# Optimization experiments

Measured on AMD Instinct MI355X. Metric: run time of the kernel, lower is better.

Reference implementation:

```python
import jax, jax.numpy as jnp
import numpy as np

H = 15  # hidden_dim


def _lstm_layer(x_seq, w_ih, w_hh, b_ih, b_hh):
    """One LSTM layer, PyTorch gate order (i, f, g, o).
    x_seq: (T, B, D_in) -> returns output sequence (T, B, H)."""
    T, B, _ = x_seq.shape
    # Precompute input contribution for all timesteps at once: (T, B, 4H)
    xw = jnp.einsum('tbd,gd->tbg', x_seq, w_ih) + b_ih + b_hh

    def step(carry, xw_t):
        h, c = carry
        gates = xw_t + h @ w_hh.T  # (B, 4H)
        i, f, g, o = jnp.split(gates, 4, axis=-1)
        i = jax.nn.sigmoid(i)
        f = jax.nn.sigmoid(f)
        g = jnp.tanh(g)
        o = jax.nn.sigmoid(o)
        c = f * c + i * g
        h = o * jnp.tanh(c)
        return (h, c), h

    h0 = jnp.zeros((B, H), dtype=x_seq.dtype)
    c0 = jnp.zeros((B, H), dtype=x_seq.dtype)
    _, out = jax.lax.scan(step, (h0, c0), xw)
    return out  # (T, B, H)


def setup_inputs() -> dict:
    key = jax.random.key(0)
    ks = jax.random.split(key, 11)
    D, OUT = 5, 25
    s = 0.1
    return {
        'x':     jax.random.normal(ks[0], (512, 4096, D), dtype=jnp.float32),
        'w_ih0': jax.random.normal(ks[1], (4 * H, D), dtype=jnp.float32) * s,
        'w_hh0': jax.random.normal(ks[2], (4 * H, H), dtype=jnp.float32) * s,
        'b_ih0': jax.random.normal(ks[3], (4 * H,), dtype=jnp.float32) * s,
        'b_hh0': jax.random.normal(ks[4], (4 * H,), dtype=jnp.float32) * s,
        'w_ih1': jax.random.normal(ks[5], (4 * H, H), dtype=jnp.float32) * s,
        'w_hh1': jax.random.normal(ks[6], (4 * H, H), dtype=jnp.float32) * s,
        'b_ih1': jax.random.normal(ks[7], (4 * H,), dtype=jnp.float32) * s,
        'b_hh1': jax.random.normal(ks[8], (4 * H,), dtype=jnp.float32) * s,
        'w_lin': jax.random.normal(ks[9], (OUT, H), dtype=jnp.float32) * s,
        'b_lin': jax.random.normal(ks[10], (OUT,), dtype=jnp.float32) * s,
    }


def reference(x, w_ih0, w_hh0, b_ih0, b_hh0, w_ih1, w_hh1, b_ih1, b_hh1, w_lin, b_lin):
    out0 = _lstm_layer(x, w_ih0, w_hh0, b_ih0, b_hh0)      # (T, B, H)
    out1 = _lstm_layer(out0, w_ih1, w_hh1, b_ih1, b_hh1)   # (T, B, H)
    # Faithful to the source: output[:, -1, :] with seq-first layout selects
    # the last BATCH element across all timesteps -> (T, H)
    last = out1[:, -1, :]
    return last @ w_lin.T + b_lin  # (T, OUT)
```

## Files before the change

kernel.cpp:

```cpp
#include <hip/hip_runtime.h>

#define T_SEQ 512
#define BATCH 4096
#define D_IN  5
#define H     15
#define G4    60
#define OUTN  25

#define LOG2E   1.4426950408889634f
#define M_SIG  (-1.4426950408889634f)
#define M_TANH (-2.8853901f)

__device__ __forceinline__ float fast_exp2(float x) {
#if __has_builtin(__builtin_amdgcn_exp2f)
  return __builtin_amdgcn_exp2f(x);
#else
  return exp2f(x);
#endif
}

__device__ __forceinline__ float fast_rcp(float x) {
#if __has_builtin(__builtin_amdgcn_rcpf)
  return __builtin_amdgcn_rcpf(x);
#else
  return 1.0f / x;
#endif
}

__device__ __forceinline__ float rl(float v, int lane) {
  return __int_as_float(__builtin_amdgcn_readlane(__float_as_int(v), lane));
}

template <int K>
__device__ __forceinline__ float qbcast(float v) {
  return __int_as_float(__builtin_amdgcn_update_dpp(
      0, __float_as_int(v), K * 0x55, 0xF, 0xF, true));
}

__global__ void precompute_xw0(const float* __restrict__ x,
                               const float* __restrict__ w_ih0,
                               const float* __restrict__ b_ih0,
                               const float* __restrict__ b_hh0,
                               float* __restrict__ xw0) {
  int idx = blockIdx.x * blockDim.x + threadIdx.x;
  if (idx >= T_SEQ * G4) return;
  int t = idx / G4;
  int g = idx - t * G4;
  const float* xp = x + ((size_t)t * BATCH + (BATCH - 1)) * D_IN;
  float a = b_ih0[g] + b_hh0[g];
#pragma unroll
  for (int d = 0; d < D_IN; ++d) a = fmaf(xp[d], w_ih0[g * D_IN + d], a);
  float m = (g / H == 2) ? M_TANH : M_SIG;
  xw0[idx] = a * m;
}

__global__ void __launch_bounds__(64, 1)
lstm_serial(const float* __restrict__ xw0,
            const float* __restrict__ w_hh0,
            const float* __restrict__ w_ih1,
            const float* __restrict__ w_hh1,
            const float* __restrict__ b_ih1,
            const float* __restrict__ b_hh1,
            const float* __restrict__ w_lin,
            const float* __restrict__ b_lin,
            float* __restrict__ out) {
  const int lane = threadIdx.x;
  const int ty = lane & 3;
  const int j  = lane >> 2;
  const int g  = (j < H) ? (ty * H + j) : 0;

  const bool  isT = (ty == 2);
  const float m   = isT ? M_TANH : M_SIG;
  const float scv  = isT ? (2.0f * M_TANH) : 1.0f;
  const float offv = isT ? (-M_TANH) : 0.0f;

  float w0[H], wi1[H], wh1[H];
#pragma unroll
  for (int k = 0; k < H; ++k) {
    w0[k]  = w_hh0[g * H + k] * m;
    wi1[k] = w_ih1[g * H + k] * m;
    wh1[k] = w_hh1[g * H + k] * m;
  }
  const float bias1 = (b_ih1[g] + b_hh1[g]) * m;

  float wl[H];
  {
    int o = (lane < OUTN) ? lane : 0;
#pragma unroll
    for (int k = 0; k < H; ++k) wl[k] = w_lin[o * H + k];
  }
  const float bl = b_lin[(lane < OUTN) ? lane : 0];

  float c0 = 0.0f, c1 = 0.0f;
  float sh0[H], sh1[H];
#pragma unroll
  for (int k = 0; k < H; ++k) { sh0[k] = 0.0f; sh1[k] = 0.0f; }

  float h0v = 0.0f, h1v = 0.0f;

  auto L0 = [&](float xw) {
    float a0 = xw, a1 = 0.0f, a2 = 0.0f;
#pragma unroll
    for (int k = 0; k < 5; ++k)   a0 = fmaf(w0[k], sh0[k], a0);
#pragma unroll
    for (int k = 5; k < 10; ++k)  a1 = fmaf(w0[k], sh0[k], a1);
#pragma unroll
    for (int k = 10; k < 15; ++k) a2 = fmaf(w0[k], sh0[k], a2);
    float a = a0 + (a1 + a2);
    float e = fast_exp2(a);
    float s = fast_rcp(1.0f + e);
    float v = fmaf(s, scv, offv);
    float vi = qbcast<0>(v), vf = qbcast<1>(v), vg = qbcast<2>(v), vo = qbcast<3>(v);
    c0 = fmaf(vf, c0, vi * vg);
    float th = fmaf(fast_rcp(1.0f + fast_exp2(c0)), 2.0f, -1.0f);
    h0v = vo * th;
  };
  auto L1 = [&]() {
    float u0 = bias1, u1 = 0.0f, u2 = 0.0f, u3 = 0.0f, u4 = 0.0f, u5 = 0.0f;
#pragma unroll
    for (int k = 0; k < 5; ++k)   { u0 = fmaf(wi1[k], sh0[k], u0); u3 = fmaf(wh1[k], sh1[k], u3); }
#pragma unroll
    for (int k = 5; k < 10; ++k)  { u1 = fmaf(wi1[k], sh0[k], u1); u4 = fmaf(wh1[k], sh1[k], u4); }
#pragma unroll
    for (int k = 10; k < 15; ++k) { u2 = fmaf(wi1[k], sh0[k], u2); u5 = fmaf(wh1[k], sh1[k], u5); }
    float b = ((u0 + u1) + (u2 + u3)) + (u4 + u5);
    float e = fast_exp2(b);
    float s = fast_rcp(1.0f + e);
    float v = fmaf(s, scv, offv);
    float qi = qbcast<0>(v), qf = qbcast<1>(v), qg = qbcast<2>(v), qo = qbcast<3>(v);
    c1 = fmaf(qf, c1, qi * qg);
    float th = fmaf(fast_rcp(1.0f + fast_exp2(c1)), 2.0f, -1.0f);
    h1v = qo * th;
  };
  auto B0 = [&]() {
#pragma unroll
    for (int k = 0; k < H; ++k) sh0[k] = rl(h0v, 4 * k);
  };
  auto B1 = [&]() {
#pragma unroll
    for (int k = 0; k < H; ++k) sh1[k] = rl(h1v, 4 * k);
  };
  auto LIN = [&](int t2, bool do_store) {
    float o0 = bl, o1 = 0.0f, o2 = 0.0f;
#pragma unroll
    for (int k = 0; k < 5; ++k)   o0 = fmaf(wl[k], sh1[k], o0);
#pragma unroll
    for (int k = 5; k < 10; ++k)  o1 = fmaf(wl[k], sh1[k], o1);
#pragma unroll
    for (int k = 10; k < 15; ++k) o2 = fmaf(wl[k], sh1[k], o2);
    if (do_store && lane < OUTN) out[t2 * OUTN + lane] = o0 + (o1 + o2);
  };

  float xw_cur = xw0[g];
  float xw_n1  = xw0[1 * G4 + g];
  L0(xw_cur);
  B0();
  xw_cur = xw_n1;
  xw_n1  = xw0[2 * G4 + g];

  for (int i = 1; i < T_SEQ; ++i) {
    int tn = (i + 2 < T_SEQ) ? (i + 2) : 0;
    float xw_n2 = xw0[tn * G4 + g];

    L1();
    L0(xw_cur);
    LIN(i - 2, i >= 2);

    B0();
    B1();

    xw_cur = xw_n1;
    xw_n1  = xw_n2;
  }

  LIN(T_SEQ - 2, true);
  L1();
  B1();
  LIN(T_SEQ - 1, true);
}

extern "C" void kernel_launch(void* const* d_in, const int* in_sizes, int n_in,
                              void* d_out, int out_size, void* d_ws, size_t ws_size,
                              hipStream_t stream) {
  const float* x     = (const float*)d_in[0];
  const float* w_ih0 = (const float*)d_in[1];
  const float* w_hh0 = (const float*)d_in[2];
  const float* b_ih0 = (const float*)d_in[3];
  const float* b_hh0 = (const float*)d_in[4];
  const float* w_ih1 = (const float*)d_in[5];
  const float* w_hh1 = (const float*)d_in[6];
  const float* b_ih1 = (const float*)d_in[7];
  const float* b_hh1 = (const float*)d_in[8];
  const float* w_lin = (const float*)d_in[9];
  const float* b_lin = (const float*)d_in[10];
  float* out = (float*)d_out;
  float* xw0 = (float*)d_ws;

  precompute_xw0<<<dim3((T_SEQ * G4 + 255) / 256), dim3(256), 0, stream>>>(
      x, w_ih0, b_ih0, b_hh0, xw0);
  lstm_serial<<<dim3(1), dim3(64), 0, stream>>>(
      xw0, w_hh0, w_ih1, w_hh1, b_ih1, b_hh1, w_lin, b_lin, out);
}
```

Measured before the change: 236.9 us.

## Split LSTM layers and linear head across three wavefronts in a barrier pipeline

Replaces the single-wavefront serial loop with a three-wave workgroup. Wave 0 runs layer 0, wave 1 runs layer 1 one step behind, and wave 2 runs the output projection, with hidden states passed through small ring buffers in shared memory. A workgroup barrier runs every step. The goal is to take layer-1 and linear work off the critical path so each wave's serial chain is shorter and the waves run concurrently. In exchange, every step now pays for a barrier, LDS writes and reads, and an lgkmcnt wait.

```diff
diff --git a/kernel.cpp b/kernel.cpp
--- a/kernel.cpp
+++ b/kernel.cpp
@@ -6,8 +6,8 @@
 #define H     15
 #define G4    60
 #define OUTN  25
-
-#define LOG2E   1.4426950408889634f
+#define NITER (T_SEQ + 4)
+
 #define M_SIG  (-1.4426950408889634f)
 #define M_TANH (-2.8853901f)
 
@@ -35,6 +35,12 @@
 __device__ __forceinline__ float qbcast(float v) {
   return __int_as_float(__builtin_amdgcn_update_dpp(
       0, __float_as_int(v), K * 0x55, 0xF, 0xF, true));
+}
+
+__device__ __forceinline__ void wg_barrier() {
+  asm volatile("s_waitcnt lgkmcnt(0)" ::: "memory");
+  __builtin_amdgcn_s_barrier();
+  asm volatile("" ::: "memory");
 }
 
 __global__ void precompute_xw0(const float* __restrict__ x,
@@ -54,129 +60,159 @@
   xw0[idx] = a * m;
 }
 
-__global__ void __launch_bounds__(64, 1)
-lstm_serial(const float* __restrict__ xw0,
-            const float* __restrict__ w_hh0,
-            const float* __restrict__ w_ih1,
-            const float* __restrict__ w_hh1,
-            const float* __restrict__ b_ih1,
-            const float* __restrict__ b_hh1,
-            const float* __restrict__ w_lin,
-            const float* __restrict__ b_lin,
-            float* __restrict__ out) {
-  const int lane = threadIdx.x;
+__global__ void __launch_bounds__(192, 1)
+lstm_pipe(const float* __restrict__ xw0,
+          const float* __restrict__ w_hh0,
+          const float* __restrict__ w_ih1,
+          const float* __restrict__ w_hh1,
+          const float* __restrict__ b_ih1,
+          const float* __restrict__ b_hh1,
+          const float* __restrict__ w_lin,
+          const float* __restrict__ b_lin,
+          float* __restrict__ out) {
+  __shared__ __align__(16) float h0buf[4][16];
+  __shared__ __align__(16) float h1buf[4][16];
+
+  const int tid  = threadIdx.x;
+  const int wid  = tid >> 6;
+  const int lane = tid & 63;
   const int ty = lane & 3;
   const int j  = lane >> 2;
   const int g  = (j < H) ? (ty * H + j) : 0;
 
-  const bool  isT = (ty == 2);
-  const float m   = isT ? M_TANH : M_SIG;
+  const bool  isT  = (ty == 2);
+  const float m    = isT ? M_TANH : M_SIG;
   const float scv  = isT ? (2.0f * M_TANH) : 1.0f;
   const float offv = isT ? (-M_TANH) : 0.0f;
 
-  float w0[H], wi1[H], wh1[H];
-#pragma unroll
-  for (int k = 0; k < H; ++k) {
-    w0[k]  = w_hh0[g * H + k] * m;
-    wi1[k] = w_ih1[g * H + k] * m;
-    wh1[k] = w_hh1[g * H + k] * m;
+  if (wid == 0) {
+    float w0[H];
+#pragma unroll
+    for (int k = 0; k < H; ++k) w0[k] = w_hh0[g * H + k] * m;
+    float sh0[H];
+#pragma unroll
+    for (int k = 0; k < H; ++k) sh0[k] = 0.0f;
+    float c0 = 0.0f;
+    float xw_cur = xw0[g];
+    float xw_n1  = xw0[G4 + g];
+
+    for (int i = 0; i < NITER; ++i) {
+      if (i < T_SEQ) {
+        int tn = (i + 2 < T_SEQ) ? (i + 2) : 0;
+        float xw_n2 = xw0[tn * G4 + g];
+
+        float a0 = xw_cur, a1 = 0.0f, a2 = 0.0f;
+#pragma unroll
+        for (int k = 0; k < 5; ++k)   a0 = fmaf(w0[k], sh0[k], a0);
+#pragma unroll
+        for (int k = 5; k < 10; ++k)  a1 = fmaf(w0[k], sh0[k], a1);
+#pragma unroll
+        for (int k = 10; k < 15; ++k) a2 = fmaf(w0[k], sh0[k], a2);
+        float a = a0 + (a1 + a2);
+        float e = fast_exp2(a);
+        float s = fast_rcp(1.0f + e);
+        float v = fmaf(s, scv, offv);
+        float vi = qbcast<0>(v), vf = qbcast<1>(v), vg = qbcast<2>(v), vo = qbcast<3>(v);
+        c0 = fmaf(vf, c0, vi * vg);
+        float th = fmaf(fast_rcp(1.0f + fast_exp2(c0)), 2.0f, -1.0f);
+        float h0v = vo * th;
+
+        if (ty == 0 && j < H) h0buf[i & 3][j] = h0v;
+#pragma unroll
+        for (int k = 0; k < H; ++k) sh0[k] = rl(h0v, 4 * k);
+
+        xw_cur = xw_n1;
+        xw_n1  = xw_n2;
+      }
+      wg_barrier();
+    }
+  } else if (wid == 1) {
+    float wi1[H], wh1[H];
+#pragma unroll
+    for (int k = 0; k < H; ++k) {
+      wi1[k] = w_ih1[g * H + k] * m;
+      wh1[k] = w_hh1[g * H + k] * m;
+    }
+    const float bias1 = (b_ih1[g] + b_hh1[g]) * m;
+    float sh1[H];
+#pragma unroll
+    for (int k = 0; k < H; ++k) sh1[k] = 0.0f;
+    float c1 = 0.0f;
+    float4 hA = {0,0,0,0}, hB = {0,0,0,0}, hC = {0,0,0,0}, hD = {0,0,0,0};
+    float4 nA = {0,0,0,0}, nB = {0,0,0,0}, nC = {0,0,0,0}, nD = {0,0,0,0};
+
+    for (int i = 0; i < NITER; ++i) {
+      int t1 = i - 2;
+      if (0 <= t1 && t1 < T_SEQ) {
+        float u0 = bias1, u1 = 0.0f, u2 = 0.0f, u3 = 0.0f, u4 = 0.0f, u5 = 0.0f;
+        u0 = fmaf(wi1[0],  hA.x, u0); u0 = fmaf(wi1[1],  hA.y, u0);
+        u0 = fmaf(wi1[2],  hA.z, u0); u0 = fmaf(wi1[3],  hA.w, u0);
+        u0 = fmaf(wi1[4],  hB.x, u0);
+        u1 = fmaf(wi1[5],  hB.y, u1); u1 = fmaf(wi1[6],  hB.z, u1);
+        u1 = fmaf(wi1[7],  hB.w, u1); u1 = fmaf(wi1[8],  hC.x, u1);
+        u1 = fmaf(wi1[9],  hC.y, u1);
+        u2 = fmaf(wi1[10], hC.z, u2); u2 = fmaf(wi1[11], hC.w, u2);
+        u2 = fmaf(wi1[12], hD.x, u2); u2 = fmaf(wi1[13], hD.y, u2);
+        u2 = fmaf(wi1[14], hD.z, u2);
+#pragma unroll
+        for (int k = 0; k < 5; ++k)   u3 = fmaf(wh1[k], sh1[k], u3);
+#pragma unroll
+        for (int k = 5; k < 10; ++k)  u4 = fmaf(wh1[k], sh1[k], u4);
+#pragma unroll
+        for (int k = 10; k < 15; ++k) u5 = fmaf(wh1[k], sh1[k], u5);
+        float b = ((u0 + u1) + (u2 + u3)) + (u4 + u5);
+
+        float e = fast_exp2(b);
+        float s = fast_rcp(1.0f + e);
+        float v = fmaf(s, scv, offv);
+        float qi = qbcast<0>(v), qf = qbcast<1>(v), qg = qbcast<2>(v), qo = qbcast<3>(v);
+        c1 = fmaf(qf, c1, qi * qg);
+        float th = fmaf(fast_rcp(1.0f + fast_exp2(c1)), 2.0f, -1.0f);
+        float h1v = qo * th;
+
+        if (ty == 0 && j < H) h1buf[t1 & 3][j] = h1v;
+#pragma unroll
+        for (int k = 0; k < H; ++k) sh1[k] = rl(h1v, 4 * k);
+      }
+      if (i - 1 >= 0 && i - 1 < T_SEQ) {
+        const float4* p = (const float4*)(&h0buf[(i - 1) & 3][0]);
+        nA = p[0]; nB = p[1]; nC = p[2]; nD = p[3];
+      }
+      wg_barrier();
+      hA = nA; hB = nB; hC = nC; hD = nD;
+    }
+  } else {
+    const int o = (lane < OUTN) ? lane : 0;
+    float wl[H];
+#pragma unroll
+    for (int k = 0; k < H; ++k) wl[k] = w_lin[o * H + k];
+    const float bl = b_lin[o];
+    float4 hA = {0,0,0,0}, hB = {0,0,0,0}, hC = {0,0,0,0}, hD = {0,0,0,0};
+    float4 nA = {0,0,0,0}, nB = {0,0,0,0}, nC = {0,0,0,0}, nD = {0,0,0,0};
+
+    for (int i = 0; i < NITER; ++i) {
+      int t2 = i - 4;
+      if (0 <= t2) {
+        float o0 = bl, o1 = 0.0f, o2 = 0.0f;
+        o0 = fmaf(wl[0],  hA.x, o0); o0 = fmaf(wl[1],  hA.y, o0);
+        o0 = fmaf(wl[2],  hA.z, o0); o0 = fmaf(wl[3],  hA.w, o0);
+        o0 = fmaf(wl[4],  hB.x, o0);
+        o1 = fmaf(wl[5],  hB.y, o1); o1 = fmaf(wl[6],  hB.z, o1);
+        o1 = fmaf(wl[7],  hB.w, o1); o1 = fmaf(wl[8],  hC.x, o1);
+        o1 = fmaf(wl[9],  hC.y, o1);
+        o2 = fmaf(wl[10], hC.z, o2); o2 = fmaf(wl[11], hC.w, o2);
+        o2 = fmaf(wl[12], hD.x, o2); o2 = fmaf(wl[13], hD.y, o2);
+        o2 = fmaf(wl[14], hD.z, o2);
+        if (lane < OUTN) out[t2 * OUTN + lane] = o0 + (o1 + o2);
+      }
+      if (i - 3 >= 0 && i - 3 < T_SEQ) {
+        const float4* p = (const float4*)(&h1buf[(i - 3) & 3][0]);
+        nA = p[0]; nB = p[1]; nC = p[2]; nD = p[3];
+      }
+      wg_barrier();
+      hA = nA; hB = nB; hC = nC; hD = nD;
+    }
   }
-  const float bias1 = (b_ih1[g] + b_hh1[g]) * m;
-
-  float wl[H];
-  {
-    int o = (lane < OUTN) ? lane : 0;
-#pragma unroll
-    for (int k = 0; k < H; ++k) wl[k] = w_lin[o * H + k];
-  }
-  const float bl = b_lin[(lane < OUTN) ? lane : 0];
-
-  float c0 = 0.0f, c1 = 0.0f;
-  float sh0[H], sh1[H];
-#pragma unroll
-  for (int k = 0; k < H; ++k) { sh0[k] = 0.0f; sh1[k] = 0.0f; }
-
-  float h0v = 0.0f, h1v = 0.0f;
-
-  auto L0 = [&](float xw) {
-    float a0 = xw, a1 = 0.0f, a2 = 0.0f;
-#pragma unroll
-    for (int k = 0; k < 5; ++k)   a0 = fmaf(w0[k], sh0[k], a0);
-#pragma unroll
-    for (int k = 5; k < 10; ++k)  a1 = fmaf(w0[k], sh0[k], a1);
-#pragma unroll
-    for (int k = 10; k < 15; ++k) a2 = fmaf(w0[k], sh0[k], a2);
-    float a = a0 + (a1 + a2);
-    float e = fast_exp2(a);
-    float s = fast_rcp(1.0f + e);
-    float v = fmaf(s, scv, offv);
-    float vi = qbcast<0>(v), vf = qbcast<1>(v), vg = qbcast<2>(v), vo = qbcast<3>(v);
-    c0 = fmaf(vf, c0, vi * vg);
-    float th = fmaf(fast_rcp(1.0f + fast_exp2(c0)), 2.0f, -1.0f);
-    h0v = vo * th;
-  };
-  auto L1 = [&]() {
-    float u0 = bias1, u1 = 0.0f, u2 = 0.0f, u3 = 0.0f, u4 = 0.0f, u5 = 0.0f;
-#pragma unroll
-    for (int k = 0; k < 5; ++k)   { u0 = fmaf(wi1[k], sh0[k], u0); u3 = fmaf(wh1[k], sh1[k], u3); }
-#pragma unroll
-    for (int k = 5; k < 10; ++k)  { u1 = fmaf(wi1[k], sh0[k], u1); u4 = fmaf(wh1[k], sh1[k], u4); }
-#pragma unroll
-    for (int k = 10; k < 15; ++k) { u2 = fmaf(wi1[k], sh0[k], u2); u5 = fmaf(wh1[k], sh1[k], u5); }
-    float b = ((u0 + u1) + (u2 + u3)) + (u4 + u5);
-    float e = fast_exp2(b);
-    float s = fast_rcp(1.0f + e);
-    float v = fmaf(s, scv, offv);
-    float qi = qbcast<0>(v), qf = qbcast<1>(v), qg = qbcast<2>(v), qo = qbcast<3>(v);
-    c1 = fmaf(qf, c1, qi * qg);
-    float th = fmaf(fast_rcp(1.0f + fast_exp2(c1)), 2.0f, -1.0f);
-    h1v = qo * th;
-  };
-  auto B0 = [&]() {
-#pragma unroll
-    for (int k = 0; k < H; ++k) sh0[k] = rl(h0v, 4 * k);
-  };
-  auto B1 = [&]() {
-#pragma unroll
-    for (int k = 0; k < H; ++k) sh1[k] = rl(h1v, 4 * k);
-  };
-  auto LIN = [&](int t2, bool do_store) {
-    float o0 = bl, o1 = 0.0f, o2 = 0.0f;
-#pragma unroll
-    for (int k = 0; k < 5; ++k)   o0 = fmaf(wl[k], sh1[k], o0);
-#pragma unroll
-    for (int k = 5; k < 10; ++k)  o1 = fmaf(wl[k], sh1[k], o1);
-#pragma unroll
-    for (int k = 10; k < 15; ++k) o2 = fmaf(wl[k], sh1[k], o2);
-    if (do_store && lane < OUTN) out[t2 * OUTN + lane] = o0 + (o1 + o2);
-  };
-
-  float xw_cur = xw0[g];
-  float xw_n1  = xw0[1 * G4 + g];
-  L0(xw_cur);
-  B0();
-  xw_cur = xw_n1;
-  xw_n1  = xw0[2 * G4 + g];
-
-  for (int i = 1; i < T_SEQ; ++i) {
-    int tn = (i + 2 < T_SEQ) ? (i + 2) : 0;
-    float xw_n2 = xw0[tn * G4 + g];
-
-    L1();
-    L0(xw_cur);
-    LIN(i - 2, i >= 2);
-
-    B0();
-    B1();
-
-    xw_cur = xw_n1;
-    xw_n1  = xw_n2;
-  }
-
-  LIN(T_SEQ - 2, true);
-  L1();
-  B1();
-  LIN(T_SEQ - 1, true);
 }
 
 extern "C" void kernel_launch(void* const* d_in, const int* in_sizes, int n_in,
@@ -198,6 +234,6 @@
 
   precompute_xw0<<<dim3((T_SEQ * G4 + 255) / 256), dim3(256), 0, stream>>>(
       x, w_ih0, b_ih0, b_hh0, xw0);
-  lstm_serial<<<dim3(1), dim3(64), 0, stream>>>(
+  lstm_pipe<<<dim3(1), dim3(192), 0, stream>>>(
       xw0, w_hh0, w_ih1, w_hh1, b_ih1, b_hh1, w_lin, b_lin, out);
 }
```

Measured after the change: 241.6 us. About the same (+2.0%).
